# Kernel tuning notes

Hardware: AMD Instinct MI355X
Metric: run time of the kernel (lower is better)

Reference implementation:

```python
import jax, jax.numpy as jnp
import numpy as np

B, NX, NY, F = 4, 4096, 4096, 16

def setup_inputs() -> dict:
    key = jax.random.key(0)
    k1, k2, k3, k4, k5 = jax.random.split(key, 5)
    return {
        "x": jax.random.normal(k1, (B, NX, 3), dtype=jnp.float32),
        "y": jax.random.normal(k2, (B, NY, 3), dtype=jnp.float32),
        "sample_x": jax.random.uniform(k3, (B, NX, F), dtype=jnp.float32),
        "sample_y": jax.random.uniform(k4, (B, NY, F), dtype=jnp.float32),
        "scale": jax.random.uniform(k5, (F,), dtype=jnp.float32),
    }

def reference(x, y, sample_x, sample_y, scale):
    sq_x = jnp.sum(x * x, axis=-1, keepdims=True)            # (B,NX,1)
    sq_y = jnp.sum(y * y, axis=-1, keepdims=True)            # (B,NY,1)
    dot = jnp.einsum('bnd,bmd->bnm', x, y)                   # (B,NX,NY)
    d = jnp.clip(sq_x + jnp.swapaxes(sq_y, -2, -1) - 2.0 * dot, 1e-10, 1e6)
    # fixed-scale branch
    s = jnp.clip(scale, 1e-6, 1e6)
    scale_x = jnp.clip(jnp.einsum('bnf,f->bn', sample_x, s), 1e-10, 1e6)  # (B,NX)
    scale_y = jnp.clip(jnp.einsum('bmf,f->bm', sample_y, s), 1e-10, 1e6)  # (B,NY)
    scale_xy = jnp.sqrt(jnp.clip(scale_x[:, :, None] * scale_y[:, None, :], 1e-10, 1e12))
    return 1.0 / (1.0 + d / scale_xy)
```

## Files before the change

### kernel.cpp

```cpp
#include <hip/hip_runtime.h>


constexpr int kB  = 4;
constexpr int kNX = 4096;
constexpr int kNY = 4096;
constexpr int kF  = 16;

__global__ __launch_bounds__(256) void row_stats_kernel(
    const float* __restrict__ x, const float* __restrict__ y,
    const float* __restrict__ sx, const float* __restrict__ sy,
    const float* __restrict__ scale,
    float2* __restrict__ rx, float2* __restrict__ ry, int nper)
{
    int t = blockIdx.x * blockDim.x + threadIdx.x;
    if (t >= 2 * nper) return;
    const float* pts; const float* smp; float2* dst; int idx;
    if (t < nper) { pts = x; smp = sx; dst = rx; idx = t; }
    else          { pts = y; smp = sy; dst = ry; idx = t - nper; }

    const float* p = pts + (size_t)idx * 3;
    float sq = p[0] * p[0] + p[1] * p[1] + p[2] * p[2];

    const float4* s4 = (const float4*)(smp + (size_t)idx * kF);
    const float4* c4 = (const float4*)scale;
    float acc = 0.f;
#pragma unroll
    for (int k = 0; k < kF / 4; ++k) {
        float4 sv = s4[k];
        float4 cv = c4[k];
        acc += sv.x * fminf(fmaxf(cv.x, 1e-6f), 1e6f);
        acc += sv.y * fminf(fmaxf(cv.y, 1e-6f), 1e6f);
        acc += sv.z * fminf(fmaxf(cv.z, 1e-6f), 1e6f);
        acc += sv.w * fminf(fmaxf(cv.w, 1e-6f), 1e6f);
    }
    float sc = fminf(fmaxf(acc, 1e-10f), 1e6f);
    dst[idx] = make_float2(sq, sc);
}

__device__ __forceinline__ void cauchy_tile(
    int b, int i0, int j0,
    const float* __restrict__ x, const float* __restrict__ y,
    const float sqx[4], const float scx[4],
    const float sqy[4], const float scy[4],
    const float xxx[4], const float xyy[4], const float xzz[4],
    const float yxx[4], const float yyy[4], const float yzz[4],
    float* __restrict__ out)
{
    size_t obase = ((size_t)b * kNX + i0) * (size_t)kNY + j0;
#pragma unroll
    for (int r = 0; r < 4; ++r) {
        float4 o;
        float* op = (float*)&o;
#pragma unroll
        for (int k = 0; k < 4; ++k) {
            float dot = xxx[r] * yxx[k] + xyy[r] * yyy[k] + xzz[r] * yzz[k];
            float d = fmaf(-2.f, dot, sqx[r] + sqy[k]);
            d = fminf(fmaxf(d, 1e-10f), 1e6f);
            float pr = fminf(fmaxf(scx[r] * scy[k], 1e-10f), 1e12f);
            float s = __builtin_amdgcn_sqrtf(pr);
            op[k] = s * __builtin_amdgcn_rcpf(s + d);
        }
        *(float4*)(out + obase + (size_t)r * kNY) = o;
    }
}

__global__ __launch_bounds__(256) void cauchy_main_kernel(
    const float* __restrict__ x, const float* __restrict__ y,
    const float2* __restrict__ rx, const float2* __restrict__ ry,
    float* __restrict__ out)
{
    const int t = blockIdx.x * 256 + threadIdx.x;
    const int jc = t & (kNY / 4 - 1);
    const int rowtile = t >> 10;
    const int b  = rowtile >> 10;
    const int i0 = (rowtile & (kNX / 4 - 1)) * 4;
    const int j0 = jc * 4;

    const float4* yv = (const float4*)(y + ((size_t)b * kNY + j0) * 3);
    float4 ya = yv[0], yb = yv[1], yc = yv[2];
    const float4* ryv = (const float4*)(ry + (size_t)b * kNY + j0);
    float4 r01 = ryv[0], r23 = ryv[1];

    const float4* xv = (const float4*)(x + ((size_t)b * kNX + i0) * 3);
    float4 xa = xv[0], xb = xv[1], xc = xv[2];
    const float4* rxv = (const float4*)(rx + (size_t)b * kNX + i0);
    float4 q01 = rxv[0], q23 = rxv[1];

    const float yxx[4] = {ya.x, ya.w, yb.z, yc.y};
    const float yyy[4] = {ya.y, yb.x, yb.w, yc.z};
    const float yzz[4] = {ya.z, yb.y, yc.x, yc.w};
    const float sqy[4] = {r01.x, r01.z, r23.x, r23.z};
    const float scy[4] = {r01.y, r01.w, r23.y, r23.w};

    const float xxx[4] = {xa.x, xa.w, xb.z, xc.y};
    const float xyy[4] = {xa.y, xb.x, xb.w, xc.z};
    const float xzz[4] = {xa.z, xb.y, xc.x, xc.w};
    const float sqx[4] = {q01.x, q01.z, q23.x, q23.z};
    const float scx[4] = {q01.y, q01.w, q23.y, q23.w};

    cauchy_tile(b, i0, j0, x, y, sqx, scx, sqy, scy,
                xxx, xyy, xzz, yxx, yyy, yzz, out);
}

__global__ __launch_bounds__(256) void cauchy_fallback_kernel(
    const float* __restrict__ x, const float* __restrict__ y,
    const float* __restrict__ sx, const float* __restrict__ sy,
    const float* __restrict__ scale, float* __restrict__ out)
{
    const int t = blockIdx.x * 256 + threadIdx.x;
    const int jc = t & (kNY / 4 - 1);
    const int rowtile = t >> 10;
    const int b  = rowtile >> 10;
    const int i0 = (rowtile & (kNX / 4 - 1)) * 4;
    const int j0 = jc * 4;

    float4 c[4];
    const float4* c4 = (const float4*)scale;
#pragma unroll
    for (int k = 0; k < 4; ++k) {
        float4 cv = c4[k];
        c[k].x = fminf(fmaxf(cv.x, 1e-6f), 1e6f);
        c[k].y = fminf(fmaxf(cv.y, 1e-6f), 1e6f);
        c[k].z = fminf(fmaxf(cv.z, 1e-6f), 1e6f);
        c[k].w = fminf(fmaxf(cv.w, 1e-6f), 1e6f);
    }

    const float4* yv = (const float4*)(y + ((size_t)b * kNY + j0) * 3);
    float4 ya = yv[0], yb = yv[1], yc = yv[2];
    const float4* xv = (const float4*)(x + ((size_t)b * kNX + i0) * 3);
    float4 xa = xv[0], xb = xv[1], xc = xv[2];

    const float yxx[4] = {ya.x, ya.w, yb.z, yc.y};
    const float yyy[4] = {ya.y, yb.x, yb.w, yc.z};
    const float yzz[4] = {ya.z, yb.y, yc.x, yc.w};
    const float xxx[4] = {xa.x, xa.w, xb.z, xc.y};
    const float xyy[4] = {xa.y, xb.x, xb.w, xc.z};
    const float xzz[4] = {xa.z, xb.y, xc.x, xc.w};

    float sqx[4], scx[4], sqy[4], scy[4];
#pragma unroll
    for (int r = 0; r < 4; ++r) {
        sqx[r] = xxx[r] * xxx[r] + xyy[r] * xyy[r] + xzz[r] * xzz[r];
        sqy[r] = yxx[r] * yxx[r] + yyy[r] * yyy[r] + yzz[r] * yzz[r];
        const float4* a4 = (const float4*)(sx + ((size_t)b * kNX + i0 + r) * kF);
        const float4* b4 = (const float4*)(sy + ((size_t)b * kNY + j0 + r) * kF);
        float accx = 0.f, accy = 0.f;
#pragma unroll
        for (int k = 0; k < 4; ++k) {
            float4 av = a4[k], bv = b4[k], cv = c[k];
            accx += av.x * cv.x + av.y * cv.y + av.z * cv.z + av.w * cv.w;
            accy += bv.x * cv.x + bv.y * cv.y + bv.z * cv.z + bv.w * cv.w;
        }
        scx[r] = fminf(fmaxf(accx, 1e-10f), 1e6f);
        scy[r] = fminf(fmaxf(accy, 1e-10f), 1e6f);
    }

    cauchy_tile(b, i0, j0, x, y, sqx, scx, sqy, scy,
                xxx, xyy, xzz, yxx, yyy, yzz, out);
}

extern "C" void kernel_launch(void* const* d_in, const int* in_sizes, int n_in,
                              void* d_out, int out_size, void* d_ws, size_t ws_size,
                              hipStream_t stream) {
    const float* x     = (const float*)d_in[0];
    const float* y     = (const float*)d_in[1];
    const float* sx    = (const float*)d_in[2];
    const float* sy    = (const float*)d_in[3];
    const float* scale = (const float*)d_in[4];
    float* out = (float*)d_out;

    const int nper = kB * kNX;
    const size_t need = (size_t)2 * nper * sizeof(float2);
    const int main_blocks = (kB * kNX * kNY / 16) / 256;

    if (ws_size >= need) {
        float2* rx = (float2*)d_ws;
        float2* ry = rx + nper;
        row_stats_kernel<<<(2 * nper + 255) / 256, 256, 0, stream>>>(
            x, y, sx, sy, scale, rx, ry, nper);
        cauchy_main_kernel<<<main_blocks, 256, 0, stream>>>(x, y, rx, ry, out);
    } else {
        cauchy_fallback_kernel<<<main_blocks, 256, 0, stream>>>(
            x, y, sx, sy, scale, out);
    }
}
```

Before: 264.7 us.

## Precompute sqrt of row scales, use 8x4 tiles and nontemporal stores

```diff
diff --git a/kernel.cpp b/kernel.cpp
--- a/kernel.cpp
+++ b/kernel.cpp
@@ -1,10 +1,13 @@
 #include <hip/hip_runtime.h>
+#include <math.h>
 
 
 constexpr int kB  = 4;
 constexpr int kNX = 4096;
 constexpr int kNY = 4096;
 constexpr int kF  = 16;
+
+typedef float f32x4 __attribute__((ext_vector_type(4)));
 
 __global__ __launch_bounds__(256) void row_stats_kernel(
     const float* __restrict__ x, const float* __restrict__ y,
@@ -34,72 +37,55 @@
         acc += sv.w * fminf(fmaxf(cv.w, 1e-6f), 1e6f);
     }
     float sc = fminf(fmaxf(acc, 1e-10f), 1e6f);
-    dst[idx] = make_float2(sq, sc);
-}
-
-__device__ __forceinline__ void cauchy_tile(
-    int b, int i0, int j0,
-    const float* __restrict__ x, const float* __restrict__ y,
-    const float sqx[4], const float scx[4],
-    const float sqy[4], const float scy[4],
-    const float xxx[4], const float xyy[4], const float xzz[4],
-    const float yxx[4], const float yyy[4], const float yzz[4],
-    float* __restrict__ out)
-{
-    size_t obase = ((size_t)b * kNX + i0) * (size_t)kNY + j0;
-#pragma unroll
-    for (int r = 0; r < 4; ++r) {
-        float4 o;
-        float* op = (float*)&o;
-#pragma unroll
-        for (int k = 0; k < 4; ++k) {
-            float dot = xxx[r] * yxx[k] + xyy[r] * yyy[k] + xzz[r] * yzz[k];
-            float d = fmaf(-2.f, dot, sqx[r] + sqy[k]);
-            d = fminf(fmaxf(d, 1e-10f), 1e6f);
-            float pr = fminf(fmaxf(scx[r] * scy[k], 1e-10f), 1e12f);
-            float s = __builtin_amdgcn_sqrtf(pr);
-            op[k] = s * __builtin_amdgcn_rcpf(s + d);
-        }
-        *(float4*)(out + obase + (size_t)r * kNY) = o;
-    }
+    dst[idx] = make_float2(sq, sqrtf(sc));
 }
 
 __global__ __launch_bounds__(256) void cauchy_main_kernel(
-    const float* __restrict__ x, const float* __restrict__ y,
-    const float2* __restrict__ rx, const float2* __restrict__ ry,
+    const float* __restrict__ x, const float2* __restrict__ rx,
+    const float* __restrict__ y, const float2* __restrict__ ry,
     float* __restrict__ out)
 {
     const int t = blockIdx.x * 256 + threadIdx.x;
     const int jc = t & (kNY / 4 - 1);
     const int rowtile = t >> 10;
-    const int b  = rowtile >> 10;
-    const int i0 = (rowtile & (kNX / 4 - 1)) * 4;
+    const int b  = rowtile >> 9;
+    const int i0 = (rowtile & (kNX / 8 - 1)) * 8;
     const int j0 = jc * 4;
 
+    float yco[12];
     const float4* yv = (const float4*)(y + ((size_t)b * kNY + j0) * 3);
-    float4 ya = yv[0], yb = yv[1], yc = yv[2];
+#pragma unroll
+    for (int k = 0; k < 3; ++k) *(float4*)(yco + 4 * k) = yv[k];
+    float2 rys[4];
     const float4* ryv = (const float4*)(ry + (size_t)b * kNY + j0);
-    float4 r01 = ryv[0], r23 = ryv[1];
+    *(float4*)(&rys[0]) = ryv[0];
+    *(float4*)(&rys[2]) = ryv[1];
 
+    float xco[24];
     const float4* xv = (const float4*)(x + ((size_t)b * kNX + i0) * 3);
-    float4 xa = xv[0], xb = xv[1], xc = xv[2];
+#pragma unroll
+    for (int k = 0; k < 6; ++k) *(float4*)(xco + 4 * k) = xv[k];
+    float2 rxs[8];
     const float4* rxv = (const float4*)(rx + (size_t)b * kNX + i0);
-    float4 q01 = rxv[0], q23 = rxv[1];
+#pragma unroll
+    for (int k = 0; k < 4; ++k) *(float4*)(&rxs[2 * k]) = rxv[k];
 
-    const float yxx[4] = {ya.x, ya.w, yb.z, yc.y};
-    const float yyy[4] = {ya.y, yb.x, yb.w, yc.z};
-    const float yzz[4] = {ya.z, yb.y, yc.x, yc.w};
-    const float sqy[4] = {r01.x, r01.z, r23.x, r23.z};
-    const float scy[4] = {r01.y, r01.w, r23.y, r23.w};
-
-    const float xxx[4] = {xa.x, xa.w, xb.z, xc.y};
-    const float xyy[4] = {xa.y, xb.x, xb.w, xc.z};
-    const float xzz[4] = {xa.z, xb.y, xc.x, xc.w};
-    const float sqx[4] = {q01.x, q01.z, q23.x, q23.z};
-    const float scx[4] = {q01.y, q01.w, q23.y, q23.w};
-
-    cauchy_tile(b, i0, j0, x, y, sqx, scx, sqy, scy,
-                xxx, xyy, xzz, yxx, yyy, yzz, out);
+    const size_t obase = ((size_t)b * kNX + i0) * (size_t)kNY + j0;
+#pragma unroll
+    for (int r = 0; r < 8; ++r) {
+        const float px = xco[3 * r], py = xco[3 * r + 1], pz = xco[3 * r + 2];
+        const float sqx = rxs[r].x, rsx = rxs[r].y;
+        f32x4 o;
+#pragma unroll
+        for (int k = 0; k < 4; ++k) {
+            float dot = px * yco[3 * k] + py * yco[3 * k + 1] + pz * yco[3 * k + 2];
+            float d = fmaf(-2.f, dot, sqx + rys[k].x);
+            d = fminf(fmaxf(d, 1e-10f), 1e6f);
+            float s = rsx * rys[k].y;
+            o[k] = s * __builtin_amdgcn_rcpf(s + d);
+        }
+        __builtin_nontemporal_store(o, (f32x4*)(out + obase + (size_t)r * kNY));
+    }
 }
 
 __global__ __launch_bounds__(256) void cauchy_fallback_kernel(
@@ -125,23 +111,19 @@
         c[k].w = fminf(fmaxf(cv.w, 1e-6f), 1e6f);
     }
 
+    float yco[12], xco[12];
     const float4* yv = (const float4*)(y + ((size_t)b * kNY + j0) * 3);
-    float4 ya = yv[0], yb = yv[1], yc = yv[2];
+#pragma unroll
+    for (int k = 0; k < 3; ++k) *(float4*)(yco + 4 * k) = yv[k];
     const float4* xv = (const float4*)(x + ((size_t)b * kNX + i0) * 3);
-    float4 xa = xv[0], xb = xv[1], xc = xv[2];
+#pragma unroll
+    for (int k = 0; k < 3; ++k) *(float4*)(xco + 4 * k) = xv[k];
 
-    const float yxx[4] = {ya.x, ya.w, yb.z, yc.y};
-    const float yyy[4] = {ya.y, yb.x, yb.w, yc.z};
-    const float yzz[4] = {ya.z, yb.y, yc.x, yc.w};
-    const float xxx[4] = {xa.x, xa.w, xb.z, xc.y};
-    const float xyy[4] = {xa.y, xb.x, xb.w, xc.z};
-    const float xzz[4] = {xa.z, xb.y, xc.x, xc.w};
-
-    float sqx[4], scx[4], sqy[4], scy[4];
+    float sqx[4], rsx[4], sqy[4], rsy[4];
 #pragma unroll
     for (int r = 0; r < 4; ++r) {
-        sqx[r] = xxx[r] * xxx[r] + xyy[r] * xyy[r] + xzz[r] * xzz[r];
-        sqy[r] = yxx[r] * yxx[r] + yyy[r] * yyy[r] + yzz[r] * yzz[r];
+        sqx[r] = xco[3*r]*xco[3*r] + xco[3*r+1]*xco[3*r+1] + xco[3*r+2]*xco[3*r+2];
+        sqy[r] = yco[3*r]*yco[3*r] + yco[3*r+1]*yco[3*r+1] + yco[3*r+2]*yco[3*r+2];
         const float4* a4 = (const float4*)(sx + ((size_t)b * kNX + i0 + r) * kF);
         const float4* b4 = (const float4*)(sy + ((size_t)b * kNY + j0 + r) * kF);
         float accx = 0.f, accy = 0.f;
@@ -151,12 +133,26 @@
             accx += av.x * cv.x + av.y * cv.y + av.z * cv.z + av.w * cv.w;
             accy += bv.x * cv.x + bv.y * cv.y + bv.z * cv.z + bv.w * cv.w;
         }
-        scx[r] = fminf(fmaxf(accx, 1e-10f), 1e6f);
-        scy[r] = fminf(fmaxf(accy, 1e-10f), 1e6f);
+        rsx[r] = sqrtf(fminf(fmaxf(accx, 1e-10f), 1e6f));
+        rsy[r] = sqrtf(fminf(fmaxf(accy, 1e-10f), 1e6f));
     }
 
-    cauchy_tile(b, i0, j0, x, y, sqx, scx, sqy, scy,
-                xxx, xyy, xzz, yxx, yyy, yzz, out);
+    const size_t obase = ((size_t)b * kNX + i0) * (size_t)kNY + j0;
+#pragma unroll
+    for (int r = 0; r < 4; ++r) {
+        float4 o;
+        float* op = (float*)&o;
+#pragma unroll
+        for (int k = 0; k < 4; ++k) {
+            float dot = xco[3*r] * yco[3*k] + xco[3*r+1] * yco[3*k+1]
+                      + xco[3*r+2] * yco[3*k+2];
+            float d = fmaf(-2.f, dot, sqx[r] + sqy[k]);
+            d = fminf(fmaxf(d, 1e-10f), 1e6f);
+            float s = rsx[r] * rsy[k];
+            op[k] = s * __builtin_amdgcn_rcpf(s + d);
+        }
+        *(float4*)(out + obase + (size_t)r * kNY) = o;
+    }
 }
 
 extern "C" void kernel_launch(void* const* d_in, const int* in_sizes, int n_in,
@@ -171,16 +167,17 @@
 
     const int nper = kB * kNX;
     const size_t need = (size_t)2 * nper * sizeof(float2);
-    const int main_blocks = (kB * kNX * kNY / 16) / 256;
 
     if (ws_size >= need) {
         float2* rx = (float2*)d_ws;
         float2* ry = rx + nper;
         row_stats_kernel<<<(2 * nper + 255) / 256, 256, 0, stream>>>(
             x, y, sx, sy, scale, rx, ry, nper);
-        cauchy_main_kernel<<<main_blocks, 256, 0, stream>>>(x, y, rx, ry, out);
+        const int main_blocks = (kB * kNX * kNY / 32) / 256;
+        cauchy_main_kernel<<<main_blocks, 256, 0, stream>>>(x, rx, y, ry, out);
     } else {
-        cauchy_fallback_kernel<<<main_blocks, 256, 0, stream>>>(
+        const int fb_blocks = (kB * kNX * kNY / 16) / 256;
+        cauchy_fallback_kernel<<<fb_blocks, 256, 0, stream>>>(
             x, y, sx, sy, scale, out);
     }
 }
```

After: 279.7 us. 5.7% more time.
